# Kernel tuning notes

Hardware: AMD Instinct MI355X
Metric: run time of the kernel (lower is better)

Reference implementation:

```python
import jax, jax.numpy as jnp
from jax import lax
import numpy as np

L, B, D_IN, D_OUT, D_MLP = 64, 32, 512, 512, 128
WINDOWS = [1, 3]
FEATS = [256, 128]
C = sum(FEATS)  # 384
EPS = 1e-5


def _leaky(x):
    return jnp.where(x >= 0, x, 0.1 * x)


def setup_inputs() -> dict:
    key = jax.random.key(0)
    ks = jax.random.split(key, 16)
    s = lambda k, shp: (jax.random.normal(k, shp, jnp.float32) * 0.02)
    inp = {}
    inp["x"] = jax.random.normal(ks[0], (L, B, D_IN), jnp.float32)
    inp["xs_mask"] = jnp.ones((L, B), jnp.float32)
    # conv + batchnorm params per window
    inp["conv_w0"] = s(ks[1], (FEATS[0], 1, D_IN * WINDOWS[0]))
    inp["conv_b0"] = jnp.zeros((FEATS[0],), jnp.float32)
    inp["gamma0"] = jnp.ones((FEATS[0],), jnp.float32)
    inp["beta0"] = jnp.zeros((FEATS[0],), jnp.float32)
    inp["conv_w1"] = s(ks[2], (FEATS[1], 1, D_IN * WINDOWS[1]))
    inp["conv_b1"] = jnp.zeros((FEATS[1],), jnp.float32)
    inp["gamma1"] = jnp.ones((FEATS[1],), jnp.float32)
    inp["beta1"] = jnp.zeros((FEATS[1],), jnp.float32)
    inp["w0"] = s(ks[3], (2 * C, D_MLP)); inp["b0"] = jnp.zeros((D_MLP,), jnp.float32)
    inp["w1"] = s(ks[4], (D_MLP, D_MLP)); inp["b1"] = jnp.zeros((D_MLP,), jnp.float32)
    inp["w2"] = s(ks[5], (D_MLP, D_MLP)); inp["b2"] = jnp.zeros((D_MLP,), jnp.float32)
    inp["w3"] = s(ks[6], (D_MLP, D_MLP)); inp["b3"] = jnp.zeros((D_MLP,), jnp.float32)
    # output MLP: Linear(d_mlp->d_mlp), Linear(d_mlp->d_out)
    inp["w4"] = s(ks[7], (D_MLP, D_MLP)); inp["b4"] = jnp.zeros((D_MLP,), jnp.float32)
    inp["w5"] = s(ks[8], (D_MLP, D_OUT)); inp["b5"] = jnp.zeros((D_OUT,), jnp.float32)
    return inp


def reference(x, xs_mask, conv_w0, conv_b0, gamma0, beta0, conv_w1, conv_b1,
              gamma1, beta1, w0, b0, w1, b1, w2, b2, w3, b3, w4, b4, w5, b5):
    # x: (L, B, E)
    x = x * xs_mask[:, :, None]
    xf = jnp.transpose(x, (1, 0, 2)).reshape(B, 1, L * D_IN)  # (B, 1, L*E)

    # CNN front-end: Conv1d(stride=d_in) + BatchNorm1d (batch stats) + LeakyReLU
    feats = []
    for win, cw, cb, g, bt in [(WINDOWS[0], conv_w0, conv_b0, gamma0, beta0),
                               (WINDOWS[1], conv_w1, conv_b1, gamma1, beta1)]:
        pad = (win - 1) // 2 * D_IN
        y = lax.conv_general_dilated(xf, cw, window_strides=(D_IN,),
                                     padding=[(pad, pad)],
                                     dimension_numbers=("NCH", "OIH", "NCH"))
        y = y + cb[None, :, None]  # (B, C_k, L)
        m = y.mean(axis=(0, 2))
        v = y.var(axis=(0, 2))  # biased var, as torch BN training mode
        y = (y - m[None, :, None]) / jnp.sqrt(v[None, :, None] + EPS)
        y = y * g[None, :, None] + bt[None, :, None]
        feats.append(_leaky(y))
    h = jnp.concatenate(feats, axis=1)          # (B, C, L)
    h = jnp.transpose(h, (2, 0, 1))             # (L, B, C)
    h = h * xs_mask[:, :, None]

    # Graph propagation: pairwise concat + first linear, split over concat halves
    # cat([h_i, h_j]) @ w0 == h_i @ w0[:C] + h_j @ w0[C:]  (avoids (L,L,B,2C) tensor)
    a = jnp.einsum("lbc,cd->lbd", h, w0[:C])    # (L, B, d_mlp)
    bb = jnp.einsum("lbc,cd->lbd", h, w0[C:])   # (L, B, d_mlp)
    p = _leaky(a[:, None, :, :] + bb[None, :, :, :] + b0)  # (L, L, B, d_mlp)
    p = _leaky(p @ w1 + b1)
    p = _leaky(p @ w2 + b2)
    p = _leaky(p @ w3 + b3)
    p = p * xs_mask[:, None, :, None]
    p = p.mean(axis=1)                          # (L, B, d_mlp)

    out = _leaky(p @ w4 + b4)
    out = _leaky(out @ w5 + b5)                 # (L, B, d_out)
    return out * xs_mask[:, :, None]
```

## Files before the change

kernel.cpp:

```cpp
#include <hip/hip_runtime.h>


#define BB 32
#define CCH 384

__device__ __forceinline__ float leaky(float x) { return fmaxf(x, 0.1f * x); }

typedef _Float16 f16x8 __attribute__((ext_vector_type(8)));
typedef float f32x4 __attribute__((ext_vector_type(4)));

union F8 { uint4 q; f16x8 h; };
union H2 { _Float16 f[2]; uint32_t u; };

__device__ __forceinline__ void split2(float d0, float d1,
                                       uint32_t& hw, uint32_t& lw) {
  H2 h, l;
  h.f[0] = (_Float16)d0; h.f[1] = (_Float16)d1;
  l.f[0] = (_Float16)((d0 - (float)h.f[0]) * 2048.0f);
  l.f[1] = (_Float16)((d1 - (float)h.f[1]) * 2048.0f);
  hw = h.u; lw = l.u;
}

__global__ __launch_bounds__(256) void conv_kernel(
    const float* __restrict__ x, const float* __restrict__ mask,
    const float* __restrict__ cw0, const float* __restrict__ cw1,
    const float* __restrict__ w1, const float* __restrict__ w2,
    const float* __restrict__ w3,
    float* __restrict__ yG, float* __restrict__ Ssum, float* __restrict__ Ssq,
    uint32_t* __restrict__ wpk)
{
  int bx = blockIdx.x;
  int tid = threadIdx.x;
  if (bx >= 256) {
    int e = (bx - 256) * 256 + tid;
    int L = e >> 13;
    int r = e & 8191;
    int k2 = r >> 7, n = r & 127;
    int k = k2 * 2;
    const float* w = (L == 0) ? w1 : (L == 1) ? w2 : w3;
    uint32_t hw, lw;
    split2(w[k * 128 + n], w[(k + 1) * 128 + n], hw, lw);
    wpk[L * 8192 + n * 64 + k2] = hw;
    wpk[24576 + L * 8192 + n * 64 + k2] = lw;
    return;
  }

  __shared__ uint32_t Ah[64 * 68], Al[64 * 68];
  __shared__ uint32_t Bh[64 * 68], Bl[64 * 68];

  int wid = __builtin_amdgcn_readfirstlane(tid >> 6);
  int lane = tid & 63;
  int m16 = lane & 15, q = lane >> 4;

  if (bx < 128) {
    int nb = bx & 3, mb = bx >> 2;
    int n0 = nb * 64;
    int row0 = mb * 64;
    const float* wbase = cw0 + n0 * 512;
    int wm = wid & 1, wn2 = wid >> 1;

    f32x4 hi[2][2], cr[2][2];
#pragma unroll
    for (int a = 0; a < 2; ++a)
#pragma unroll
      for (int b = 0; b < 2; ++b) {
        hi[a][b] = (f32x4){0.f, 0.f, 0.f, 0.f};
        cr[a][b] = (f32x4){0.f, 0.f, 0.f, 0.f};
      }

#pragma unroll 1
    for (int ch = 0; ch < 4; ++ch) {
      int kg0 = ch * 128;
      __syncthreads();
#pragma unroll 1
      for (int it = 0; it < 4; ++it) {
        int idx = it * 256 + tid;
        int r = idx >> 4;
        int k8 = (idx & 15) * 8;
        float d[8];
        int rowg = row0 + r;
        {
          float mv = mask[rowg];
          const float* xp = x + rowg * 512 + kg0 + k8;
          float4 a0 = *(const float4*)xp;
          float4 a1 = *(const float4*)(xp + 4);
          d[0] = a0.x * mv; d[1] = a0.y * mv; d[2] = a0.z * mv; d[3] = a0.w * mv;
          d[4] = a1.x * mv; d[5] = a1.y * mv; d[6] = a1.z * mv; d[7] = a1.w * mv;
        }
        uint4 hq, lq;
        split2(d[0], d[1], hq.x, lq.x);
        split2(d[2], d[3], hq.y, lq.y);
        split2(d[4], d[5], hq.z, lq.z);
        split2(d[6], d[7], hq.w, lq.w);
        *(uint4*)&Ah[r * 68 + k8 / 2] = hq;
        *(uint4*)&Al[r * 68 + k8 / 2] = lq;
        const float* wp = wbase + r * 512 + kg0 + k8;
        float4 b0v = *(const float4*)wp;
        float4 b1v = *(const float4*)(wp + 4);
        split2(b0v.x, b0v.y, hq.x, lq.x);
        split2(b0v.z, b0v.w, hq.y, lq.y);
        split2(b1v.x, b1v.y, hq.z, lq.z);
        split2(b1v.z, b1v.w, hq.w, lq.w);
        *(uint4*)&Bh[r * 68 + k8 / 2] = hq;
        *(uint4*)&Bl[r * 68 + k8 / 2] = lq;
      }
      __syncthreads();
#pragma unroll
      for (int ks = 0; ks < 4; ++ks) {
        int koff = ks * 16 + q * 4;
        F8 bh[2], bl[2];
#pragma unroll
        for (int nt = 0; nt < 2; ++nt) {
          int br = wn2 * 32 + nt * 16 + m16;
          bh[nt].q = *(const uint4*)&Bh[br * 68 + koff];
          bl[nt].q = *(const uint4*)&Bl[br * 68 + koff];
        }
#pragma unroll
        for (int mt = 0; mt < 2; ++mt) {
          int ar = wm * 32 + mt * 16 + m16;
          F8 ah, al;
          ah.q = *(const uint4*)&Ah[ar * 68 + koff];
          al.q = *(const uint4*)&Al[ar * 68 + koff];
#pragma unroll
          for (int nt = 0; nt < 2; ++nt) {
            hi[mt][nt] = __builtin_amdgcn_mfma_f32_16x16x32_f16(
                ah.h, bh[nt].h, hi[mt][nt], 0, 0, 0);
            cr[mt][nt] = __builtin_amdgcn_mfma_f32_16x16x32_f16(
                ah.h, bl[nt].h, cr[mt][nt], 0, 0, 0);
            cr[mt][nt] = __builtin_amdgcn_mfma_f32_16x16x32_f16(
                al.h, bh[nt].h, cr[mt][nt], 0, 0, 0);
          }
        }
      }
    }

    float y[2][2][4];
#pragma unroll
    for (int mt = 0; mt < 2; ++mt)
#pragma unroll
      for (int nt = 0; nt < 2; ++nt)
#pragma unroll
        for (int rg = 0; rg < 4; ++rg)
          y[mt][nt][rg] = hi[mt][nt][rg] + cr[mt][nt][rg] * (1.0f / 2048.0f);

#pragma unroll
    for (int nt = 0; nt < 2; ++nt) {
      float s = 0.f, s2 = 0.f;
#pragma unroll
      for (int mt = 0; mt < 2; ++mt)
#pragma unroll
        for (int rg = 0; rg < 4; ++rg) {
          float v = y[mt][nt][rg];
          s += v; s2 += v * v;
        }
      s  += __shfl_xor(s, 16, 64);  s  += __shfl_xor(s, 32, 64);
      s2 += __shfl_xor(s2, 16, 64); s2 += __shfl_xor(s2, 32, 64);
      if (lane < 16) {
        int c = n0 + wn2 * 32 + nt * 16 + m16;
        atomicAdd(&Ssum[c], s);
        atomicAdd(&Ssq[c], s2);
      }
    }

    __syncthreads();
    float* Yl = (float*)Ah;
#pragma unroll
    for (int mt = 0; mt < 2; ++mt)
#pragma unroll
      for (int nt = 0; nt < 2; ++nt)
#pragma unroll
        for (int rg = 0; rg < 4; ++rg)
          Yl[(wn2 * 32 + nt * 16 + m16) * 68 + wm * 32 + mt * 16 + q * 4 + rg] =
              y[mt][nt][rg];
    __syncthreads();
    {
      int c = tid >> 2, seg = (tid & 3) * 16;
#pragma unroll
      for (int j = 0; j < 16; j += 4)
        *(float4*)&yG[(n0 + c) * 2048 + row0 + seg + j] =
            *(const float4*)&Yl[c * 68 + seg + j];
    }
    return;
  }

  {
    int t = bx - 128;
    int nb3 = t & 1, mb3 = t >> 1;
    int n0 = 256 + nb3 * 64;
    int row0 = mb3 * 32;
    const float* wbase = cw1 + (n0 - 256) * 1536;

    f32x4 hi3[2], cr3[2];
#pragma unroll
    for (int mt = 0; mt < 2; ++mt) {
      hi3[mt] = (f32x4){0.f, 0.f, 0.f, 0.f};
      cr3[mt] = (f32x4){0.f, 0.f, 0.f, 0.f};
    }

#pragma unroll 1
    for (int ch = 0; ch < 12; ++ch) {
      int kg0 = ch * 128;
      int tap = kg0 >> 9;
      int d0 = kg0 & 511;
      int shift = (tap - 1) * 32;
      __syncthreads();
#pragma unroll 1
      for (int it = 0; it < 6; ++it) {
        int idx = it * 256 + tid;
        if (idx < 512) {
          int r = idx >> 4;
          int k8 = (idx & 15) * 8;
          float d[8];
          int rowg = row0 + r + shift;
          if ((unsigned)rowg < 2048u) {
            float mv = mask[rowg];
            const float* xp = x + rowg * 512 + d0 + k8;
            float4 a0 = *(const float4*)xp;
            float4 a1 = *(const float4*)(xp + 4);
            d[0] = a0.x * mv; d[1] = a0.y * mv; d[2] = a0.z * mv; d[3] = a0.w * mv;
            d[4] = a1.x * mv; d[5] = a1.y * mv; d[6] = a1.z * mv; d[7] = a1.w * mv;
          } else {
#pragma unroll
            for (int t2 = 0; t2 < 8; ++t2) d[t2] = 0.f;
          }
          uint4 hq, lq;
          split2(d[0], d[1], hq.x, lq.x);
          split2(d[2], d[3], hq.y, lq.y);
          split2(d[4], d[5], hq.z, lq.z);
          split2(d[6], d[7], hq.w, lq.w);
          *(uint4*)&Ah[r * 68 + k8 / 2] = hq;
          *(uint4*)&Al[r * 68 + k8 / 2] = lq;
        } else {
          int idx2 = idx - 512;
          int r = idx2 >> 4;
          int k8 = (idx2 & 15) * 8;
          const float* wp = wbase + r * 1536 + kg0 + k8;
          float4 b0v = *(const float4*)wp;
          float4 b1v = *(const float4*)(wp + 4);
          uint4 hq, lq;
          split2(b0v.x, b0v.y, hq.x, lq.x);
          split2(b0v.z, b0v.w, hq.y, lq.y);
          split2(b1v.x, b1v.y, hq.z, lq.z);
          split2(b1v.z, b1v.w, hq.w, lq.w);
          *(uint4*)&Bh[r * 68 + k8 / 2] = hq;
          *(uint4*)&Bl[r * 68 + k8 / 2] = lq;
        }
      }
      __syncthreads();
#pragma unroll
      for (int ks = 0; ks < 4; ++ks) {
        int koff = ks * 16 + q * 4;
        F8 bh, bl;
        int br = wid * 16 + m16;
        bh.q = *(const uint4*)&Bh[br * 68 + koff];
        bl.q = *(const uint4*)&Bl[br * 68 + koff];
#pragma unroll
        for (int mt = 0; mt < 2; ++mt) {
          int ar = mt * 16 + m16;
          F8 ah, al;
          ah.q = *(const uint4*)&Ah[ar * 68 + koff];
          al.q = *(const uint4*)&Al[ar * 68 + koff];
          hi3[mt] = __builtin_amdgcn_mfma_f32_16x16x32_f16(
              ah.h, bh.h, hi3[mt], 0, 0, 0);
          cr3[mt] = __builtin_amdgcn_mfma_f32_16x16x32_f16(
              ah.h, bl.h, cr3[mt], 0, 0, 0);
          cr3[mt] = __builtin_amdgcn_mfma_f32_16x16x32_f16(
              al.h, bh.h, cr3[mt], 0, 0, 0);
        }
      }
    }

    float y3[2][4];
#pragma unroll
    for (int mt = 0; mt < 2; ++mt)
#pragma unroll
      for (int rg = 0; rg < 4; ++rg)
        y3[mt][rg] = hi3[mt][rg] + cr3[mt][rg] * (1.0f / 2048.0f);

    {
      float s = 0.f, s2 = 0.f;
#pragma unroll
      for (int mt = 0; mt < 2; ++mt)
#pragma unroll
        for (int rg = 0; rg < 4; ++rg) {
          float v = y3[mt][rg];
          s += v; s2 += v * v;
        }
      s  += __shfl_xor(s, 16, 64);  s  += __shfl_xor(s, 32, 64);
      s2 += __shfl_xor(s2, 16, 64); s2 += __shfl_xor(s2, 32, 64);
      if (lane < 16) {
        int c = n0 + wid * 16 + m16;
        atomicAdd(&Ssum[c], s);
        atomicAdd(&Ssq[c], s2);
      }
    }

    __syncthreads();
    float* Yl = (float*)Ah;
#pragma unroll
    for (int mt = 0; mt < 2; ++mt)
#pragma unroll
      for (int rg = 0; rg < 4; ++rg)
        Yl[(wid * 16 + m16) * 34 + mt * 16 + q * 4 + rg] = y3[mt][rg];
    __syncthreads();
    {
      int c = tid >> 2, seg = (tid & 3) * 8;
#pragma unroll
      for (int j = 0; j < 8; j += 4)
        *(float4*)&yG[(n0 + c) * 2048 + row0 + seg + j] =
            *(const float4*)&Yl[c * 34 + seg + j];
    }
  }
}

__global__ __launch_bounds__(256) void ab_kernel(
    const float* __restrict__ yG, const float* __restrict__ Ssum,
    const float* __restrict__ Ssq,
    const float* __restrict__ g0, const float* __restrict__ be0,
    const float* __restrict__ g1, const float* __restrict__ be1,
    const float* __restrict__ mask, const float* __restrict__ w0,
    float* __restrict__ a_arr, float* __restrict__ bb_arr)
{
  int bx = blockIdx.x;
  int tid = threadIdx.x;
  __shared__ float As[64 * 20];
  __shared__ float Ws[64 * 68];
  __shared__ float scs[384], shs[384];
  for (int c = tid; c < 384; c += 256) {
    float Sv = Ssum[c], S2v = Ssq[c];
    float mean = Sv * (1.f / 2048.f);
    float var  = S2v * (1.f / 2048.f) - mean * mean;
    float g  = (c < 256) ? g0[c] : g1[c - 256];
    float be = (c < 256) ? be0[c] : be1[c - 256];
    float sc = g / sqrtf(var + 1e-5f);
    scs[c] = sc;
    shs[c] = be - mean * sc;
  }
  __syncthreads();

  int rt = bx >> 2, ct = bx & 3;
  int row0 = rt * 16, n0 = ct * 64;
  int cth = tid >> 2;
  int srr4 = (tid & 3) * 4;
  int wn16 = (tid & 3) * 16;
  int r4 = (tid >> 6) * 4;
  int n1 = tid & 63;
  const float* wbase = (n0 < 128) ? (w0 + n0) : (w0 + CCH * 128 + (n0 - 128));
  float4 mv = *(const float4*)(mask + row0 + srr4);

  float acc[4] = {0.f, 0.f, 0.f, 0.f};
#pragma unroll 1
  for (int c0 = 0; c0 < 384; c0 += 64) {
    int c = c0 + cth;
    float4 yv = *(const float4*)(yG + c * 2048 + row0 + srr4);
    float sc = scs[c], sh = shs[c];
    float4 wv0 = *(const float4*)(wbase + c * 128 + wn16);
    float4 wv1 = *(const float4*)(wbase + c * 128 + wn16 + 4);
    float4 wv2 = *(const float4*)(wbase + c * 128 + wn16 + 8);
    float4 wv3 = *(const float4*)(wbase + c * 128 + wn16 + 12);
    __syncthreads();
    float4 hv;
    hv.x = leaky(fmaf(yv.x, sc, sh)) * mv.x;
    hv.y = leaky(fmaf(yv.y, sc, sh)) * mv.y;
    hv.z = leaky(fmaf(yv.z, sc, sh)) * mv.z;
    hv.w = leaky(fmaf(yv.w, sc, sh)) * mv.w;
    *(float4*)&As[cth * 20 + srr4] = hv;
    *(float4*)&Ws[cth * 68 + wn16]      = wv0;
    *(float4*)&Ws[cth * 68 + wn16 + 4]  = wv1;
    *(float4*)&Ws[cth * 68 + wn16 + 8]  = wv2;
    *(float4*)&Ws[cth * 68 + wn16 + 12] = wv3;
    __syncthreads();
#pragma unroll 16
    for (int cc = 0; cc < 64; ++cc) {
      float4 a = *(const float4*)&As[cc * 20 + r4];
      float w  = Ws[cc * 68 + n1];
      acc[0] = fmaf(a.x, w, acc[0]);
      acc[1] = fmaf(a.y, w, acc[1]);
      acc[2] = fmaf(a.z, w, acc[2]);
      acc[3] = fmaf(a.w, w, acc[3]);
    }
  }
  float* dst; int nd;
  if (n0 < 128) { dst = a_arr; nd = n0; } else { dst = bb_arr; nd = n0 - 128; }
#pragma unroll
  for (int ri = 0; ri < 4; ++ri)
    dst[(row0 + r4 + ri) * 128 + nd + n1] = acc[ri];
}

__global__ __launch_bounds__(512) void pair_kernel(
    const float* __restrict__ a_arr, const float* __restrict__ bb_arr,
    const float* __restrict__ b0, const uint32_t* __restrict__ wpk,
    const float* __restrict__ b1, const float* __restrict__ b2,
    const float* __restrict__ b3, const float* __restrict__ mask,
    float* __restrict__ p_arr)
{
  __shared__ uint32_t AhsD[2][64 * 68];
  __shared__ uint32_t AlsD[2][64 * 68];
  __shared__ float Pm[128];
  int i = blockIdx.x, bp = blockIdx.y;
  int tid = threadIdx.x;
  int wid = __builtin_amdgcn_readfirstlane(tid >> 6);
  int lane = tid & 63;
  int m16 = lane & 15, q = lane >> 4;
  int wn16 = wid * 16, wrow = wn16 + m16;
  int k8 = (tid & 15) * 8;
  int r0 = tid >> 4;

  F8 Wh, Wl, Whn, Wln;
  Wh.q = *(const uint4*)(wpk + wrow * 64 + q * 4);
  Wl.q = *(const uint4*)(wpk + 24576 + wrow * 64 + q * 4);

  float zz[8];
  *(float4*)&zz[0] = *(const float4*)(b0 + k8);
  *(float4*)&zz[4] = *(const float4*)(b0 + k8 + 4);

  int bbase = bp * 8;
  int brow0 = i * BB + bbase;

  float av[8], bv[2][8];
  auto LOADB = [&](int bt) {
    const float* ap = a_arr + (i * BB + bt) * 128 + k8;
    *(float4*)&av[0] = *(const float4*)ap;
    *(float4*)&av[4] = *(const float4*)(ap + 4);
#pragma unroll
    for (int it = 0; it < 2; ++it) {
      int r = it * 32 + r0;
      const float* bbp = bb_arr + (r * BB + bt) * 128 + k8;
      *(float4*)&bv[it][0] = *(const float4*)bbp;
      *(float4*)&bv[it][4] = *(const float4*)(bbp + 4);
    }
  };
  auto WRITEB = [&](int buf) {
    uint32_t* Ah = AhsD[buf];
    uint32_t* Al = AlsD[buf];
#pragma unroll
    for (int it = 0; it < 2; ++it) {
      int r = it * 32 + r0;
      float d[8];
#pragma unroll
      for (int j = 0; j < 8; ++j) d[j] = leaky(av[j] + zz[j] + bv[it][j]);
      uint4 hq, lq;
      split2(d[0], d[1], hq.x, lq.x);
      split2(d[2], d[3], hq.y, lq.y);
      split2(d[4], d[5], hq.z, lq.z);
      split2(d[6], d[7], hq.w, lq.w);
      *(uint4*)&Ah[r * 68 + k8 / 2] = hq;
      *(uint4*)&Al[r * 68 + k8 / 2] = lq;
    }
  };

  LOADB(bbase);
  WRITEB(0);
  __syncthreads();

  f32x4 hi[4], cr[4];

#pragma unroll 1
  for (int t = 0; t < 8; ++t) {
    int browp = brow0 + t;
    if (t < 7) LOADB(bbase + t + 1);
    int cur = t & 1;
    uint32_t* Ahs = AhsD[cur];
    uint32_t* Als = AlsD[cur];

#pragma unroll 1
    for (int L = 0; L < 3; ++L) {
      const uint32_t* WhL = wpk + L * 8192;
      const uint32_t* WlL = wpk + 24576 + L * 8192;
      const float* Bv = (L == 0) ? b1 : (L == 1) ? b2 : b3;
#pragma unroll
      for (int mt = 0; mt < 4; ++mt) {
        hi[mt] = (f32x4){0.f, 0.f, 0.f, 0.f};
        cr[mt] = (f32x4){0.f, 0.f, 0.f, 0.f};
      }

#pragma unroll
      for (int ks = 0; ks < 4; ++ks) {
        int koff = ks * 16 + q * 4;
        if (ks < 3) {
          Whn.q = *(const uint4*)(WhL + wrow * 64 + koff + 16);
          Wln.q = *(const uint4*)(WlL + wrow * 64 + koff + 16);
        } else {
          const uint32_t* nh = (L < 2) ? (WhL + 8192) : wpk;
          const uint32_t* nl = (L < 2) ? (WlL + 8192) : (wpk + 24576);
          Whn.q = *(const uint4*)(nh + wrow * 64 + q * 4);
          Wln.q = *(const uint4*)(nl + wrow * 64 + q * 4);
        }
#pragma unroll
        for (int mt = 0; mt < 4; ++mt) {
          int arow = mt * 16 + m16;
          F8 Ah, Al;
          Ah.q = *(const uint4*)&Ahs[arow * 68 + koff];
          Al.q = *(const uint4*)&Als[arow * 68 + koff];
          hi[mt] = __builtin_amdgcn_mfma_f32_16x16x32_f16(
              Ah.h, Wh.h, hi[mt], 0, 0, 0);
          cr[mt] = __builtin_amdgcn_mfma_f32_16x16x32_f16(
              Ah.h, Wl.h, cr[mt], 0, 0, 0);
          cr[mt] = __builtin_amdgcn_mfma_f32_16x16x32_f16(
              Al.h, Wh.h, cr[mt], 0, 0, 0);
        }
        Wh = Whn; Wl = Wln;
      }

      float bias = Bv[wrow];

      if (L < 2) {
        __syncthreads();
        int par = lane & 1;
        int colw = (wn16 + (m16 & ~1)) >> 1;
#pragma unroll
        for (int mt = 0; mt < 4; ++mt) {
#pragma unroll
          for (int rg = 0; rg < 4; ++rg) {
            float dd = leaky(hi[mt][rg] + cr[mt][rg] * (1.0f / 2048.0f) + bias);
            float dn = __shfl_xor(dd, 1, 64);
            float de = par ? dn : dd;
            float do_ = par ? dd : dn;
            uint32_t hw, lw;
            split2(de, do_, hw, lw);
            int row = mt * 16 + q * 4 + rg;
            if (par) Als[row * 68 + colw] = lw;
            else     Ahs[row * 68 + colw] = hw;
          }
        }
        __syncthreads();
        if (L == 0 && t < 7) WRITEB(cur ^ 1);
      } else {
        float s = 0.f;
#pragma unroll
        for (int mt = 0; mt < 4; ++mt)
#pragma unroll
          for (int rg = 0; rg < 4; ++rg)
            s += leaky(hi[mt][rg] + cr[mt][rg] * (1.0f / 2048.0f) + bias);
        s += __shfl_xor(s, 16, 64);
        s += __shfl_xor(s, 32, 64);
        float mfac = (1.0f / 64.0f) * mask[browp];
        __syncthreads();
        if (lane < 16) Pm[wrow] = s * mfac;
        __syncthreads();
        if (tid < 128) p_arr[browp * 128 + tid] = Pm[tid];
      }
    }
  }
}

__global__ __launch_bounds__(256) void out_kernel(
    const float* __restrict__ p_arr,
    const float* __restrict__ w4, const float* __restrict__ b4,
    const float* __restrict__ w5, const float* __restrict__ b5,
    const float* __restrict__ mask, float* __restrict__ out)
{
  __shared__ float Ps[8 * 128];
  __shared__ float Ts[8 * 128];
  int bx = blockIdx.x;
  int tid = threadIdx.x;
  int row0 = bx * 8;

  {
    int o = tid * 4;
    *(float4*)&Ps[o] = *(const float4*)(p_arr + row0 * 128 + o);
  }
  __syncthreads();

  {
    int o = tid * 4;
    int rr = o >> 7, cc = o & 127;
    float4 acc = *(const float4*)(b4 + cc);
    const float* pr = Ps + rr * 128;
#pragma unroll 8
    for (int c = 0; c < 128; ++c) {
      float pv = pr[c];
      float4 wv = *(const float4*)(w4 + c * 128 + cc);
      acc.x = fmaf(pv, wv.x, acc.x);
      acc.y = fmaf(pv, wv.y, acc.y);
      acc.z = fmaf(pv, wv.z, acc.z);
      acc.w = fmaf(pv, wv.w, acc.w);
    }
    float4 tv;
    tv.x = leaky(acc.x); tv.y = leaky(acc.y);
    tv.z = leaky(acc.z); tv.w = leaky(acc.w);
    *(float4*)&Ts[o] = tv;
  }
  __syncthreads();

  {
    int kk = tid * 2;
    float acc[8][2];
    float b5v0 = b5[kk], b5v1 = b5[kk + 1];
#pragma unroll
    for (int r = 0; r < 8; ++r) { acc[r][0] = b5v0; acc[r][1] = b5v1; }
#pragma unroll 4
    for (int c = 0; c < 128; ++c) {
      float2 wv = *(const float2*)(w5 + c * 512 + kk);
#pragma unroll
      for (int r = 0; r < 8; ++r) {
        float tv = Ts[r * 128 + c];
        acc[r][0] = fmaf(tv, wv.x, acc[r][0]);
        acc[r][1] = fmaf(tv, wv.y, acc[r][1]);
      }
    }
#pragma unroll
    for (int r = 0; r < 8; ++r) {
      float mk = mask[row0 + r];
      float2 ov;
      ov.x = leaky(acc[r][0]) * mk;
      ov.y = leaky(acc[r][1]) * mk;
      *(float2*)&out[(row0 + r) * 512 + kk] = ov;
    }
  }
}

extern "C" void kernel_launch(void* const* d_in, const int* in_sizes, int n_in,
                              void* d_out, int out_size, void* d_ws, size_t ws_size,
                              hipStream_t stream) {
  const float* x    = (const float*)d_in[0];
  const float* mask = (const float*)d_in[1];
  const float* cw0  = (const float*)d_in[2];
  const float* g0   = (const float*)d_in[4];
  const float* be0  = (const float*)d_in[5];
  const float* cw1  = (const float*)d_in[6];
  const float* g1   = (const float*)d_in[8];
  const float* be1  = (const float*)d_in[9];
  const float* w0   = (const float*)d_in[10];
  const float* b0   = (const float*)d_in[11];
  const float* w1   = (const float*)d_in[12];
  const float* b1   = (const float*)d_in[13];
  const float* w2   = (const float*)d_in[14];
  const float* b2   = (const float*)d_in[15];
  const float* w3   = (const float*)d_in[16];
  const float* b3   = (const float*)d_in[17];
  const float* w4   = (const float*)d_in[18];
  const float* b4   = (const float*)d_in[19];
  const float* w5   = (const float*)d_in[20];
  const float* b5   = (const float*)d_in[21];

  float* ws     = (float*)d_ws;
  float* Ssum   = ws;
  float* Ssq    = ws + 384;
  float* yG     = ws + 768;
  uint32_t* wpk = (uint32_t*)(ws + 787200);
  float* a_arr  = ws + 836352;
  float* bb_arr = ws + 1098496;
  float* p_arr  = yG;
  float* outp   = (float*)d_out;

  hipMemsetAsync(Ssum, 0, 768 * sizeof(float), stream);
  conv_kernel<<<352, 256, 0, stream>>>(x, mask, cw0, cw1, w1, w2, w3,
                                       yG, Ssum, Ssq, wpk);
  ab_kernel<<<512, 256, 0, stream>>>(yG, Ssum, Ssq, g0, be0, g1, be1,
                                     mask, w0, a_arr, bb_arr);
  dim3 g5(64, 4);
  pair_kernel<<<g5, 512, 0, stream>>>(a_arr, bb_arr, b0, wpk, b1, b2, b3,
                                      mask, p_arr);
  out_kernel<<<256, 256, 0, stream>>>(p_arr, w4, b4, w5, b5, mask, outp);
}
```

Before: 266.0 us.

## Swizzle pair-kernel LDS, drop double buffer, double grid for occupancy

Drops the double-buffered LDS tiles in the pair kernel for a single buffer, which halves shared memory, and asks for two 512-thread blocks per CU through launch bounds. The grid is doubled so each block handles four batch columns instead of eight. LDS addressing gets an XOR swizzle on 16-byte units to cut bank conflicts on the MFMA operand reads and the writeback. The next batch's tile is now written after the last layer's sync rather than overlapped, so some load and compute overlap is given up in exchange for more resident waves and more parallelism.

```diff
diff --git a/kernel.cpp b/kernel.cpp
--- a/kernel.cpp
+++ b/kernel.cpp
@@ -387,15 +387,15 @@
     dst[(row0 + r4 + ri) * 128 + nd + n1] = acc[ri];
 }
 
-__global__ __launch_bounds__(512) void pair_kernel(
+__global__ __launch_bounds__(512, 2) void pair_kernel(
     const float* __restrict__ a_arr, const float* __restrict__ bb_arr,
     const float* __restrict__ b0, const uint32_t* __restrict__ wpk,
     const float* __restrict__ b1, const float* __restrict__ b2,
     const float* __restrict__ b3, const float* __restrict__ mask,
     float* __restrict__ p_arr)
 {
-  __shared__ uint32_t AhsD[2][64 * 68];
-  __shared__ uint32_t AlsD[2][64 * 68];
+  __shared__ uint32_t Ahs[64 * 68];
+  __shared__ uint32_t Als[64 * 68];
   __shared__ float Pm[128];
   int i = blockIdx.x, bp = blockIdx.y;
   int tid = threadIdx.x;
@@ -404,6 +404,7 @@
   int m16 = lane & 15, q = lane >> 4;
   int wn16 = wid * 16, wrow = wn16 + m16;
   int k8 = (tid & 15) * 8;
+  int u0 = tid & 15;
   int r0 = tid >> 4;
 
   F8 Wh, Wl, Whn, Wln;
@@ -414,7 +415,7 @@
   *(float4*)&zz[0] = *(const float4*)(b0 + k8);
   *(float4*)&zz[4] = *(const float4*)(b0 + k8 + 4);
 
-  int bbase = bp * 8;
+  int bbase = bp * 4;
   int brow0 = i * BB + bbase;
 
   float av[8], bv[2][8];
@@ -430,9 +431,7 @@
       *(float4*)&bv[it][4] = *(const float4*)(bbp + 4);
     }
   };
-  auto WRITEB = [&](int buf) {
-    uint32_t* Ah = AhsD[buf];
-    uint32_t* Al = AlsD[buf];
+  auto WRITEB = [&]() {
 #pragma unroll
     for (int it = 0; it < 2; ++it) {
       int r = it * 32 + r0;
@@ -444,24 +443,22 @@
       split2(d[2], d[3], hq.y, lq.y);
       split2(d[4], d[5], hq.z, lq.z);
       split2(d[6], d[7], hq.w, lq.w);
-      *(uint4*)&Ah[r * 68 + k8 / 2] = hq;
-      *(uint4*)&Al[r * 68 + k8 / 2] = lq;
+      int up = r * 68 + ((u0 ^ (r & 7)) << 2);
+      *(uint4*)&Ahs[up] = hq;
+      *(uint4*)&Als[up] = lq;
     }
   };
 
   LOADB(bbase);
-  WRITEB(0);
+  WRITEB();
   __syncthreads();
 
   f32x4 hi[4], cr[4];
 
 #pragma unroll 1
-  for (int t = 0; t < 8; ++t) {
+  for (int t = 0; t < 4; ++t) {
     int browp = brow0 + t;
-    if (t < 7) LOADB(bbase + t + 1);
-    int cur = t & 1;
-    uint32_t* Ahs = AhsD[cur];
-    uint32_t* Als = AlsD[cur];
+    if (t < 3) LOADB(bbase + t + 1);
 
 #pragma unroll 1
     for (int L = 0; L < 3; ++L) {
@@ -476,8 +473,8 @@
 
 #pragma unroll
       for (int ks = 0; ks < 4; ++ks) {
-        int koff = ks * 16 + q * 4;
         if (ks < 3) {
+          int koff = ks * 16 + q * 4;
           Whn.q = *(const uint4*)(WhL + wrow * 64 + koff + 16);
           Wln.q = *(const uint4*)(WlL + wrow * 64 + koff + 16);
         } else {
@@ -489,9 +486,10 @@
 #pragma unroll
         for (int mt = 0; mt < 4; ++mt) {
           int arow = mt * 16 + m16;
+          int ru = arow * 68 + (((ks * 4 + q) ^ (arow & 7)) << 2);
           F8 Ah, Al;
-          Ah.q = *(const uint4*)&Ahs[arow * 68 + koff];
-          Al.q = *(const uint4*)&Als[arow * 68 + koff];
+          Ah.q = *(const uint4*)&Ahs[ru];
+          Al.q = *(const uint4*)&Als[ru];
           hi[mt] = __builtin_amdgcn_mfma_f32_16x16x32_f16(
               Ah.h, Wh.h, hi[mt], 0, 0, 0);
           cr[mt] = __builtin_amdgcn_mfma_f32_16x16x32_f16(
@@ -519,12 +517,12 @@
             uint32_t hw, lw;
             split2(de, do_, hw, lw);
             int row = mt * 16 + q * 4 + rg;
-            if (par) Als[row * 68 + colw] = lw;
-            else     Ahs[row * 68 + colw] = hw;
+            int addr = row * 68 + (((colw >> 2) ^ (row & 7)) << 2) + (colw & 3);
+            if (par) Als[addr] = lw;
+            else     Ahs[addr] = hw;
           }
         }
         __syncthreads();
-        if (L == 0 && t < 7) WRITEB(cur ^ 1);
       } else {
         float s = 0.f;
 #pragma unroll
@@ -536,6 +534,7 @@
         s += __shfl_xor(s, 32, 64);
         float mfac = (1.0f / 64.0f) * mask[browp];
         __syncthreads();
+        if (t < 3) WRITEB();
         if (lane < 16) Pm[wrow] = s * mfac;
         __syncthreads();
         if (tid < 128) p_arr[browp * 128 + tid] = Pm[tid];
@@ -649,7 +648,7 @@
                                        yG, Ssum, Ssq, wpk);
   ab_kernel<<<512, 256, 0, stream>>>(yG, Ssum, Ssq, g0, be0, g1, be1,
                                      mask, w0, a_arr, bb_arr);
-  dim3 g5(64, 4);
+  dim3 g5(64, 8);
   pair_kernel<<<g5, 512, 0, stream>>>(a_arr, bb_arr, b0, wpk, b1, b2, b3,
                                       mask, p_arr);
   out_kernel<<<256, 256, 0, stream>>>(p_arr, w4, b4, w5, b5, mask, outp);
```

After: 271.0 us. No clear change (+1.9%).

## Split pair kernel over j halves with one batch per block

Applied to the files above, without the earlier changes.

The pair kernel now launches 4096 blocks of 256 threads instead of 256 blocks of 512. Each block handles one (i, b) pair and half of the j range, with each wave computing a 32-column tile. This removes the 8-step sequential batch loop and its double-buffered shared memory, aiming for more blocks per CU and better latency hiding. Each j-half writes its own partial mean, and out_kernel sums the two partials. The costs are more redundant weight loads per block and a larger partial buffer at p_arr + 262144, which must fit in the workspace.

```diff
diff --git a/kernel.cpp b/kernel.cpp
--- a/kernel.cpp
+++ b/kernel.cpp
@@ -387,132 +387,140 @@
     dst[(row0 + r4 + ri) * 128 + nd + n1] = acc[ri];
 }
 
-__global__ __launch_bounds__(512) void pair_kernel(
+__global__ __launch_bounds__(256) void pair_kernel(
     const float* __restrict__ a_arr, const float* __restrict__ bb_arr,
     const float* __restrict__ b0, const uint32_t* __restrict__ wpk,
     const float* __restrict__ b1, const float* __restrict__ b2,
     const float* __restrict__ b3, const float* __restrict__ mask,
     float* __restrict__ p_arr)
 {
-  __shared__ uint32_t AhsD[2][64 * 68];
-  __shared__ uint32_t AlsD[2][64 * 68];
+  __shared__ uint32_t Ahs[32 * 68];
+  __shared__ uint32_t Als[32 * 68];
   __shared__ float Pm[128];
-  int i = blockIdx.x, bp = blockIdx.y;
+  int i = blockIdx.x;
+  int b = blockIdx.y & 31, jh = blockIdx.y >> 5;
   int tid = threadIdx.x;
   int wid = __builtin_amdgcn_readfirstlane(tid >> 6);
   int lane = tid & 63;
   int m16 = lane & 15, q = lane >> 4;
-  int wn16 = wid * 16, wrow = wn16 + m16;
-  int k8 = (tid & 15) * 8;
-  int r0 = tid >> 4;
-
-  F8 Wh, Wl, Whn, Wln;
-  Wh.q = *(const uint4*)(wpk + wrow * 64 + q * 4);
-  Wl.q = *(const uint4*)(wpk + 24576 + wrow * 64 + q * 4);
-
-  float zz[8];
-  *(float4*)&zz[0] = *(const float4*)(b0 + k8);
-  *(float4*)&zz[4] = *(const float4*)(b0 + k8 + 4);
-
-  int bbase = bp * 8;
-  int brow0 = i * BB + bbase;
-
-  float av[8], bv[2][8];
-  auto LOADB = [&](int bt) {
-    const float* ap = a_arr + (i * BB + bt) * 128 + k8;
-    *(float4*)&av[0] = *(const float4*)ap;
-    *(float4*)&av[4] = *(const float4*)(ap + 4);
+  int browp = i * BB + b;
+
+  int col0 = wid * 32;
+  int wc[2];
+  wc[0] = col0 + m16;
+  wc[1] = col0 + 16 + m16;
+
+  F8 Wh[2], Wl[2], Whn[2], Wln[2];
+#pragma unroll
+  for (int nt = 0; nt < 2; ++nt) {
+    Wh[nt].q = *(const uint4*)(wpk + wc[nt] * 64 + q * 4);
+    Wl[nt].q = *(const uint4*)(wpk + 24576 + wc[nt] * 64 + q * 4);
+  }
+
+  {
+    int k8 = (tid & 15) * 8;
+    const float* ap = a_arr + browp * 128 + k8;
+    const float* zp = b0 + k8;
+    float az[8];
+#pragma unroll
+    for (int t = 0; t < 8; t += 4) {
+      float4 av = *(const float4*)(ap + t);
+      float4 zv = *(const float4*)(zp + t);
+      az[t + 0] = av.x + zv.x; az[t + 1] = av.y + zv.y;
+      az[t + 2] = av.z + zv.z; az[t + 3] = av.w + zv.w;
+    }
 #pragma unroll
     for (int it = 0; it < 2; ++it) {
-      int r = it * 32 + r0;
-      const float* bbp = bb_arr + (r * BB + bt) * 128 + k8;
-      *(float4*)&bv[it][0] = *(const float4*)bbp;
-      *(float4*)&bv[it][4] = *(const float4*)(bbp + 4);
-    }
-  };
-  auto WRITEB = [&](int buf) {
-    uint32_t* Ah = AhsD[buf];
-    uint32_t* Al = AlsD[buf];
-#pragma unroll
-    for (int it = 0; it < 2; ++it) {
-      int r = it * 32 + r0;
+      int r = it * 16 + (tid >> 4);
+      int j = jh * 32 + r;
+      const float* bbp = bb_arr + (j * BB + b) * 128 + k8;
       float d[8];
 #pragma unroll
-      for (int j = 0; j < 8; ++j) d[j] = leaky(av[j] + zz[j] + bv[it][j]);
+      for (int t = 0; t < 8; t += 4) {
+        float4 bv = *(const float4*)(bbp + t);
+        d[t + 0] = leaky(az[t + 0] + bv.x);
+        d[t + 1] = leaky(az[t + 1] + bv.y);
+        d[t + 2] = leaky(az[t + 2] + bv.z);
+        d[t + 3] = leaky(az[t + 3] + bv.w);
+      }
       uint4 hq, lq;
       split2(d[0], d[1], hq.x, lq.x);
       split2(d[2], d[3], hq.y, lq.y);
       split2(d[4], d[5], hq.z, lq.z);
       split2(d[6], d[7], hq.w, lq.w);
-      *(uint4*)&Ah[r * 68 + k8 / 2] = hq;
-      *(uint4*)&Al[r * 68 + k8 / 2] = lq;
-    }
-  };
-
-  LOADB(bbase);
-  WRITEB(0);
+      *(uint4*)&Ahs[r * 68 + k8 / 2] = hq;
+      *(uint4*)&Als[r * 68 + k8 / 2] = lq;
+    }
+  }
   __syncthreads();
 
-  f32x4 hi[4], cr[4];
+  f32x4 hi[2][2], cr[2][2];
 
 #pragma unroll 1
-  for (int t = 0; t < 8; ++t) {
-    int browp = brow0 + t;
-    if (t < 7) LOADB(bbase + t + 1);
-    int cur = t & 1;
-    uint32_t* Ahs = AhsD[cur];
-    uint32_t* Als = AlsD[cur];
-
-#pragma unroll 1
-    for (int L = 0; L < 3; ++L) {
-      const uint32_t* WhL = wpk + L * 8192;
-      const uint32_t* WlL = wpk + 24576 + L * 8192;
-      const float* Bv = (L == 0) ? b1 : (L == 1) ? b2 : b3;
-#pragma unroll
-      for (int mt = 0; mt < 4; ++mt) {
-        hi[mt] = (f32x4){0.f, 0.f, 0.f, 0.f};
-        cr[mt] = (f32x4){0.f, 0.f, 0.f, 0.f};
-      }
-
-#pragma unroll
-      for (int ks = 0; ks < 4; ++ks) {
-        int koff = ks * 16 + q * 4;
-        if (ks < 3) {
-          Whn.q = *(const uint4*)(WhL + wrow * 64 + koff + 16);
-          Wln.q = *(const uint4*)(WlL + wrow * 64 + koff + 16);
-        } else {
-          const uint32_t* nh = (L < 2) ? (WhL + 8192) : wpk;
-          const uint32_t* nl = (L < 2) ? (WlL + 8192) : (wpk + 24576);
-          Whn.q = *(const uint4*)(nh + wrow * 64 + q * 4);
-          Wln.q = *(const uint4*)(nl + wrow * 64 + q * 4);
-        }
-#pragma unroll
-        for (int mt = 0; mt < 4; ++mt) {
-          int arow = mt * 16 + m16;
-          F8 Ah, Al;
-          Ah.q = *(const uint4*)&Ahs[arow * 68 + koff];
-          Al.q = *(const uint4*)&Als[arow * 68 + koff];
-          hi[mt] = __builtin_amdgcn_mfma_f32_16x16x32_f16(
-              Ah.h, Wh.h, hi[mt], 0, 0, 0);
-          cr[mt] = __builtin_amdgcn_mfma_f32_16x16x32_f16(
-              Ah.h, Wl.h, cr[mt], 0, 0, 0);
-          cr[mt] = __builtin_amdgcn_mfma_f32_16x16x32_f16(
-              Al.h, Wh.h, cr[mt], 0, 0, 0);
-        }
-        Wh = Whn; Wl = Wln;
-      }
-
-      float bias = Bv[wrow];
-
-      if (L < 2) {
-        __syncthreads();
-        int par = lane & 1;
-        int colw = (wn16 + (m16 & ~1)) >> 1;
-#pragma unroll
-        for (int mt = 0; mt < 4; ++mt) {
+  for (int L = 0; L < 3; ++L) {
+    const uint32_t* WhL = wpk + L * 8192;
+    const uint32_t* WlL = wpk + 24576 + L * 8192;
+    const float* Bv = (L == 0) ? b1 : (L == 1) ? b2 : b3;
+#pragma unroll
+    for (int mt = 0; mt < 2; ++mt)
+#pragma unroll
+      for (int nt = 0; nt < 2; ++nt) {
+        hi[mt][nt] = (f32x4){0.f, 0.f, 0.f, 0.f};
+        cr[mt][nt] = (f32x4){0.f, 0.f, 0.f, 0.f};
+      }
+
+#pragma unroll
+    for (int ks = 0; ks < 4; ++ks) {
+      int koff = ks * 16 + q * 4;
+      if (ks < 3) {
+#pragma unroll
+        for (int nt = 0; nt < 2; ++nt) {
+          Whn[nt].q = *(const uint4*)(WhL + wc[nt] * 64 + koff + 16);
+          Wln[nt].q = *(const uint4*)(WlL + wc[nt] * 64 + koff + 16);
+        }
+      } else if (L < 2) {
+#pragma unroll
+        for (int nt = 0; nt < 2; ++nt) {
+          Whn[nt].q = *(const uint4*)(WhL + 8192 + wc[nt] * 64 + q * 4);
+          Wln[nt].q = *(const uint4*)(WlL + 8192 + wc[nt] * 64 + q * 4);
+        }
+      }
+#pragma unroll
+      for (int mt = 0; mt < 2; ++mt) {
+        int arow = mt * 16 + m16;
+        F8 Ah, Al;
+        Ah.q = *(const uint4*)&Ahs[arow * 68 + koff];
+        Al.q = *(const uint4*)&Als[arow * 68 + koff];
+#pragma unroll
+        for (int nt = 0; nt < 2; ++nt) {
+          hi[mt][nt] = __builtin_amdgcn_mfma_f32_16x16x32_f16(
+              Ah.h, Wh[nt].h, hi[mt][nt], 0, 0, 0);
+          cr[mt][nt] = __builtin_amdgcn_mfma_f32_16x16x32_f16(
+              Ah.h, Wl[nt].h, cr[mt][nt], 0, 0, 0);
+          cr[mt][nt] = __builtin_amdgcn_mfma_f32_16x16x32_f16(
+              Al.h, Wh[nt].h, cr[mt][nt], 0, 0, 0);
+        }
+      }
+#pragma unroll
+      for (int nt = 0; nt < 2; ++nt) { Wh[nt] = Whn[nt]; Wl[nt] = Wln[nt]; }
+    }
+
+    float bias[2];
+#pragma unroll
+    for (int nt = 0; nt < 2; ++nt) bias[nt] = Bv[wc[nt]];
+
+    if (L < 2) {
+      __syncthreads();
+      int par = lane & 1;
+#pragma unroll
+      for (int mt = 0; mt < 2; ++mt) {
+#pragma unroll
+        for (int nt = 0; nt < 2; ++nt) {
+          int colw = (col0 + nt * 16 + (m16 & ~1)) >> 1;
 #pragma unroll
           for (int rg = 0; rg < 4; ++rg) {
-            float dd = leaky(hi[mt][rg] + cr[mt][rg] * (1.0f / 2048.0f) + bias);
+            float dd = leaky(hi[mt][nt][rg] + cr[mt][nt][rg] * (1.0f / 2048.0f)
+                             + bias[nt]);
             float dn = __shfl_xor(dd, 1, 64);
             float de = par ? dn : dd;
             float do_ = par ? dd : dn;
@@ -523,23 +531,32 @@
             else     Ahs[row * 68 + colw] = hw;
           }
         }
-        __syncthreads();
-        if (L == 0 && t < 7) WRITEB(cur ^ 1);
-      } else {
-        float s = 0.f;
-#pragma unroll
-        for (int mt = 0; mt < 4; ++mt)
+      }
+      __syncthreads();
+    } else {
+      float s[2] = {0.f, 0.f};
+#pragma unroll
+      for (int nt = 0; nt < 2; ++nt)
+#pragma unroll
+        for (int mt = 0; mt < 2; ++mt)
 #pragma unroll
           for (int rg = 0; rg < 4; ++rg)
-            s += leaky(hi[mt][rg] + cr[mt][rg] * (1.0f / 2048.0f) + bias);
-        s += __shfl_xor(s, 16, 64);
-        s += __shfl_xor(s, 32, 64);
-        float mfac = (1.0f / 64.0f) * mask[browp];
-        __syncthreads();
-        if (lane < 16) Pm[wrow] = s * mfac;
-        __syncthreads();
-        if (tid < 128) p_arr[browp * 128 + tid] = Pm[tid];
-      }
+            s[nt] += leaky(hi[mt][nt][rg] + cr[mt][nt][rg] * (1.0f / 2048.0f)
+                           + bias[nt]);
+      float mfac = (1.0f / 64.0f) * mask[browp];
+#pragma unroll
+      for (int nt = 0; nt < 2; ++nt) {
+        s[nt] += __shfl_xor(s[nt], 16, 64);
+        s[nt] += __shfl_xor(s[nt], 32, 64);
+      }
+      if (lane < 16) {
+#pragma unroll
+        for (int nt = 0; nt < 2; ++nt)
+          Pm[col0 + nt * 16 + m16] = s[nt] * mfac;
+      }
+      __syncthreads();
+      if (tid < 128)
+        p_arr[(jh * 2048 + browp) * 128 + tid] = Pm[tid];
     }
   }
 }
@@ -558,7 +575,12 @@
 
   {
     int o = tid * 4;
-    *(float4*)&Ps[o] = *(const float4*)(p_arr + row0 * 128 + o);
+    float4 p0 = *(const float4*)(p_arr + row0 * 128 + o);
+    float4 p1 = *(const float4*)(p_arr + 262144 + row0 * 128 + o);
+    float4 pv;
+    pv.x = p0.x + p1.x; pv.y = p0.y + p1.y;
+    pv.z = p0.z + p1.z; pv.w = p0.w + p1.w;
+    *(float4*)&Ps[o] = pv;
   }
   __syncthreads();
 
@@ -649,8 +671,8 @@
                                        yG, Ssum, Ssq, wpk);
   ab_kernel<<<512, 256, 0, stream>>>(yG, Ssum, Ssq, g0, be0, g1, be1,
                                      mask, w0, a_arr, bb_arr);
-  dim3 g5(64, 4);
-  pair_kernel<<<g5, 512, 0, stream>>>(a_arr, bb_arr, b0, wpk, b1, b2, b3,
+  dim3 g5(64, 64);
+  pair_kernel<<<g5, 256, 0, stream>>>(a_arr, bb_arr, b0, wpk, b1, b2, b3,
                                       mask, p_arr);
   out_kernel<<<256, 256, 0, stream>>>(p_arr, w4, b4, w5, b5, mask, outp);
 }
```

Measured after the change: 277.0 us. +4.1%, slower.
